# Kernel tuning notes

Hardware: AMD Instinct MI355X
Metric: run time of the kernel (lower is better)

The kernel has to match this reference:

```python
import jax, jax.numpy as jnp
import numpy as np

# Longformer/Lawformer-style encoder: sliding-window local attention (one-sided
# window W) + G global tokens (CLS), pooler, 2-class linear head, CE loss.
B, S, D, H, DH, L, W, G = 2, 4096, 768, 12, 64, 2, 128, 1
DFF, VOCAB = 3072, 50265
NEG = -3e4  # masked-score fill, safe in fp16/bf16/fp32


def layernorm(x, g, b):
    mu = x.mean(-1, keepdims=True)
    var = ((x - mu) ** 2).mean(-1, keepdims=True)
    return (x - mu) * jax.lax.rsqrt(var + 1e-5) * g + b


def setup_inputs() -> dict:
    key = jax.random.key(0)
    ks = iter(jax.random.split(key, 64))
    nrm = lambda shape: jax.random.normal(next(ks), shape, jnp.float32) * 0.02
    inp = {
        'inputx': jax.random.randint(next(ks), (B, S), 0, VOCAB),
        'mask': jnp.ones((B, S), jnp.float32),
        'labels': jax.random.randint(next(ks), (B,), 0, 2),
        'tok_emb': nrm((VOCAB, D)),
        'pos_emb': nrm((S, D)),
        'ln_emb_g': jnp.ones((D,)), 'ln_emb_b': jnp.zeros((D,)),
        'Wq': nrm((L, D, D)), 'bq': jnp.zeros((L, D)),
        'Wk': nrm((L, D, D)), 'bk': jnp.zeros((L, D)),
        'Wv': nrm((L, D, D)), 'bv': jnp.zeros((L, D)),
        'Wqg': nrm((L, D, D)), 'bqg': jnp.zeros((L, D)),
        'Wkg': nrm((L, D, D)), 'bkg': jnp.zeros((L, D)),
        'Wvg': nrm((L, D, D)), 'bvg': jnp.zeros((L, D)),
        'Wo': nrm((L, D, D)), 'bo': jnp.zeros((L, D)),
        'ln1_g': jnp.ones((L, D)), 'ln1_b': jnp.zeros((L, D)),
        'W1': nrm((L, D, DFF)), 'b1': jnp.zeros((L, DFF)),
        'W2': nrm((L, DFF, D)), 'b2': jnp.zeros((L, D)),
        'ln2_g': jnp.ones((L, D)), 'ln2_b': jnp.zeros((L, D)),
        'Wp': nrm((D, D)), 'bp': jnp.zeros((D,)),
        'Wfc': nrm((D, 2)), 'bfc': jnp.zeros((2,)),
    }
    return inp


def reference(inputx, mask, labels, tok_emb, pos_emb, ln_emb_g, ln_emb_b,
              Wq, bq, Wk, bk, Wv, bv, Wqg, bqg, Wkg, bkg, Wvg, bvg,
              Wo, bo, ln1_g, ln1_b, W1, b1, W2, b2, ln2_g, ln2_b,
              Wp, bp, Wfc, bfc):
    x = tok_emb[inputx] + pos_emb[None]          # [B,S,D]
    x = layernorm(x, ln_emb_g, ln_emb_b)
    nb = S // W
    scale = 1.0 / np.sqrt(DH)
    # static band validity mask: query i attends keys in [i-W, i+W]
    qi = jnp.arange(W)[:, None]                   # [W,1]
    ki = jnp.arange(3 * W)[None, :]               # [1,3W]
    band = (ki >= qi) & (ki <= qi + 2 * W)        # [W,3W]
    kpos = (jnp.arange(nb)[:, None, None] - 1) * W + ki[None]  # [nb,1,3W]
    band_mask = band[None] & (kpos >= G) & (kpos < S)           # [nb,W,3W]; global keys handled separately

    def heads(t):
        return t.reshape(B, S, H, DH).transpose(0, 2, 1, 3)  # [B,H,S,DH]

    for l in range(L):
        q = heads(x @ Wq[l] + bq[l]) * scale
        k = heads(x @ Wk[l] + bk[l])
        v = heads(x @ Wv[l] + bv[l])
        qg = heads(x @ Wqg[l] + bqg[l]) * scale
        kg = heads(x @ Wkg[l] + bkg[l])
        vg = heads(x @ Wvg[l] + bvg[l])
        # --- local banded attention via 3-block gather ---
        kb = k.reshape(B, H, nb, W, DH)
        vb = v.reshape(B, H, nb, W, DH)
        kp = jnp.pad(kb, ((0, 0), (0, 0), (1, 1), (0, 0), (0, 0)))
        vp = jnp.pad(vb, ((0, 0), (0, 0), (1, 1), (0, 0), (0, 0)))
        k3 = jnp.concatenate([kp[:, :, :-2], kp[:, :, 1:-1], kp[:, :, 2:]], axis=3)  # [B,H,nb,3W,DH]
        v3 = jnp.concatenate([vp[:, :, :-2], vp[:, :, 1:-1], vp[:, :, 2:]], axis=3)
        mb = mask.reshape(B, nb, W)
        mp = jnp.pad(mb, ((0, 0), (1, 1), (0, 0)))
        m3 = jnp.concatenate([mp[:, :-2], mp[:, 1:-1], mp[:, 2:]], axis=2)  # [B,nb,3W]
        sc = jnp.einsum('bhnqd,bhnkd->bhnqk', q.reshape(B, H, nb, W, DH), k3)  # [B,H,nb,W,3W]
        ok = band_mask[None, None] & (m3[:, None, :, None, :] > 0)
        sc = jnp.where(ok, sc, NEG)
        # --- every token also attends to the G global tokens (global k/v proj) ---
        scg = jnp.einsum('bhsd,bhgd->bhsg', q, kg[:, :, :G])
        scg = jnp.where(mask[:, None, None, :G] > 0, scg, NEG)
        all_sc = jnp.concatenate([scg, sc.reshape(B, H, S, 3 * W)], axis=-1)  # [B,H,S,G+3W]
        p = jax.nn.softmax(all_sc, axis=-1)
        pg = p[..., :G]
        pb = p[..., G:].reshape(B, H, nb, W, 3 * W)
        out = jnp.einsum('bhnqk,bhnkd->bhnqd', pb, v3).reshape(B, H, S, DH)
        out = out + jnp.einsum('bhsg,bhgd->bhsd', pg, vg[:, :, :G])
        # --- global tokens: full attention over all S with global projections ---
        scf = jnp.einsum('bhgd,bhsd->bhgs', qg[:, :, :G], kg)
        scf = jnp.where(mask[:, None, None, :] > 0, scf, NEG)
        outg = jnp.einsum('bhgs,bhsd->bhgd', jax.nn.softmax(scf, axis=-1), vg)
        out = out.at[:, :, :G].set(outg)
        out = out.transpose(0, 2, 1, 3).reshape(B, S, D) @ Wo[l] + bo[l]
        x = layernorm(x + out, ln1_g[l], ln1_b[l])
        h = jax.nn.gelu(x @ W1[l] + b1[l])
        x = layernorm(x + h @ W2[l] + b2[l], ln2_g[l], ln2_b[l])
    pooled = jnp.tanh(x[:, 0] @ Wp + bp)          # pooler_output
    logits = pooled @ Wfc + bfc                   # [B,2]
    logp = jax.nn.log_softmax(logits, axis=-1)
    loss = -jnp.mean(jnp.take_along_axis(logp, labels[:, None], axis=1))
    return loss
```

## Files before the change

### kernel.cpp

```cpp
#include <hip/hip_runtime.h>
#include <hip/hip_bf16.h>
#include <math.h>

#define B_    2
#define S_    4096
#define D_    768
#define H_    12
#define DH_   64
#define L_    2
#define W_    128
#define G_    1
#define DFF_  3072
#define NEG_  (-30000.0f)
#define NROWS (B_ * S_)
#define ST5   (5 * D_)
#define QOFF  0
#define KOFF  (1 * D_)
#define VOFF  (2 * D_)
#define KGOFF (3 * D_)
#define VGOFF (4 * D_)
#define QPB   64
#define CHK   32

typedef __attribute__((ext_vector_type(8))) unsigned short bfrag;
typedef __attribute__((ext_vector_type(4))) float f32x4;

__device__ __forceinline__ unsigned short f2bf(float f) {
  __hip_bfloat16 h = __float2bfloat16(f);
  return *reinterpret_cast<unsigned short*>(&h);
}

__device__ __forceinline__ void gload16(const void* g, void* l) {
  __builtin_amdgcn_global_load_lds(
      (const __attribute__((address_space(1))) unsigned int*)g,
      (__attribute__((address_space(3))) unsigned int*)l, 16, 0, 0);
}

__device__ __forceinline__ float wave_sum(float v) {
#pragma unroll
  for (int o = 32; o > 0; o >>= 1) v += __shfl_down(v, o, 64);
  return v;
}
__device__ __forceinline__ float wave_max(float v) {
#pragma unroll
  for (int o = 32; o > 0; o >>= 1) v = fmaxf(v, __shfl_down(v, o, 64));
  return v;
}
__device__ __forceinline__ float block_sum256(float v, float* sbuf) {
  v = wave_sum(v);
  int lane = threadIdx.x & 63, wid = threadIdx.x >> 6;
  if (lane == 0) sbuf[wid] = v;
  __syncthreads();
  float r = sbuf[0] + sbuf[1] + sbuf[2] + sbuf[3];
  __syncthreads();
  return r;
}

__device__ __forceinline__ float gelu_f(float x) {
  const float c = 0.7978845608028654f;
  float x3 = x * x * x;
  return 0.5f * x * (1.0f + tanhf(c * (x + 0.044715f * x3)));
}

__global__ __launch_bounds__(256) void embed_ln_kernel(
    const int* __restrict__ inputx, const float* __restrict__ tok_emb,
    const float* __restrict__ pos_emb, const float* __restrict__ g,
    const float* __restrict__ bta, float* __restrict__ X,
    unsigned short* __restrict__ Xbf) {
  __shared__ float sbuf[4];
  int row = blockIdx.x;
  int s = row & (S_ - 1);
  int tok = inputx[row];
  const float* te = tok_emb + (size_t)tok * D_;
  const float* pe = pos_emb + (size_t)s * D_;
  float vals[3];
#pragma unroll
  for (int i = 0; i < 3; i++) {
    int d = threadIdx.x + i * 256;
    vals[i] = te[d] + pe[d];
  }
  float tot = block_sum256(vals[0] + vals[1] + vals[2], sbuf);
  float mu = tot * (1.0f / D_);
  float sq = 0.f;
#pragma unroll
  for (int i = 0; i < 3; i++) { float c = vals[i] - mu; sq += c * c; }
  float var = block_sum256(sq, sbuf) * (1.0f / D_);
  float rs = rsqrtf(var + 1e-5f);
  float* xr = X + (size_t)row * D_;
  unsigned short* xb = Xbf + (size_t)row * D_;
#pragma unroll
  for (int i = 0; i < 3; i++) {
    int d = threadIdx.x + i * 256;
    float v = (vals[i] - mu) * rs * g[d] + bta[d];
    xr[d] = v;
    xb[d] = f2bf(v);
  }
}

__global__ __launch_bounds__(256) void add_ln_kernel(
    const float* __restrict__ Xin, const float* __restrict__ T,
    const float* __restrict__ g, const float* __restrict__ bta,
    float* __restrict__ Xout, unsigned short* __restrict__ Xbf) {
  __shared__ float sbuf[4];
  int row = blockIdx.x;
  const float* xr = Xin + (size_t)row * D_;
  const float* tr = T + (size_t)row * D_;
  float vals[3];
#pragma unroll
  for (int i = 0; i < 3; i++) {
    int d = threadIdx.x + i * 256;
    vals[i] = xr[d] + tr[d];
  }
  float tot = block_sum256(vals[0] + vals[1] + vals[2], sbuf);
  float mu = tot * (1.0f / D_);
  float sq = 0.f;
#pragma unroll
  for (int i = 0; i < 3; i++) { float c = vals[i] - mu; sq += c * c; }
  float var = block_sum256(sq, sbuf) * (1.0f / D_);
  float rs = rsqrtf(var + 1e-5f);
  float* xo = Xout + (size_t)row * D_;
  unsigned short* xb = Xbf + (size_t)row * D_;
#pragma unroll
  for (int i = 0; i < 3; i++) {
    int d = threadIdx.x + i * 256;
    float v = (vals[i] - mu) * rs * g[d] + bta[d];
    xo[d] = v;
    xb[d] = f2bf(v);
  }
}

__global__ __launch_bounds__(256) void wtrans_kernel(
    const float* __restrict__ W, unsigned short* __restrict__ WT, int K, int N) {
  __shared__ float tile[32][33];
  int n0 = blockIdx.x * 32, k0 = blockIdx.y * 32;
  int tx = threadIdx.x & 31, ty = threadIdx.x >> 5;
#pragma unroll
  for (int i = 0; i < 4; i++) {
    int r = ty + i * 8;
    tile[r][tx] = W[(size_t)(k0 + r) * N + n0 + tx];
  }
  __syncthreads();
#pragma unroll
  for (int i = 0; i < 4; i++) {
    int r = ty + i * 8;
    WT[(size_t)(n0 + r) * K + k0 + tx] = f2bf(tile[tx][r]);
  }
}

__global__ __launch_bounds__(256) void bias_pack_kernel(
    const float* __restrict__ bq, const float* __restrict__ bk,
    const float* __restrict__ bv, const float* __restrict__ bkg,
    const float* __restrict__ bvg, float* __restrict__ bias5) {
  int l = blockIdx.y;
  int j = blockIdx.x * 256 + threadIdx.x;
  if (j >= ST5) return;
  int which = j / D_, r = j - which * D_;
  float v;
  switch (which) {
    case 0: v = bq[l * D_ + r]; break;
    case 1: v = bk[l * D_ + r]; break;
    case 2: v = bv[l * D_ + r]; break;
    case 3: v = bkg[l * D_ + r]; break;
    default: v = bvg[l * D_ + r]; break;
  }
  bias5[(size_t)l * ST5 + j] = v;
}

__global__ __launch_bounds__(256) void gemm_bf16_kernel(
    const unsigned short* __restrict__ A, const unsigned short* __restrict__ BT,
    const float* __restrict__ bias, float* __restrict__ C,
    unsigned short* __restrict__ Cbf, int M, int N, int K, int mode) {
  __shared__ __align__(16) unsigned short As[128 * 32];
  __shared__ __align__(16) unsigned short Bs[128 * 32];
  const int m0 = blockIdx.y * 128, n0 = blockIdx.x * 128;
  const int t = threadIdx.x;
  const int w = t >> 6, l = t & 63;
  const int wm = w >> 1, wn = w & 1;
  const int lr = l & 15, lg = l >> 4;
  f32x4 acc[4][4] = {};
  for (int k0 = 0; k0 < K; k0 += 32) {
    __syncthreads();
#pragma unroll
    for (int i = 0; i < 2; i++) {
      int idx = t + i * 256;
      int row = idx >> 2, c = idx & 3;
      gload16(&A[(size_t)(m0 + row) * K + k0 + c * 8], &As[idx * 8]);
      gload16(&BT[(size_t)(n0 + row) * K + k0 + c * 8], &Bs[idx * 8]);
    }
    __syncthreads();
    bfrag af[4], bf[4];
#pragma unroll
    for (int f = 0; f < 4; f++) {
      int ra = wm * 64 + f * 16 + lr;
      af[f] = *reinterpret_cast<const bfrag*>(&As[ra * 32 + lg * 8]);
      int rb = wn * 64 + f * 16 + lr;
      bf[f] = *reinterpret_cast<const bfrag*>(&Bs[rb * 32 + lg * 8]);
    }
#pragma unroll
    for (int mi = 0; mi < 4; mi++)
#pragma unroll
      for (int ni = 0; ni < 4; ni++)
        asm volatile("v_mfma_f32_16x16x32_bf16 %0, %1, %2, %0"
                     : "+v"(acc[mi][ni])
                     : "v"(af[mi]), "v"(bf[ni]));
  }
  asm volatile("s_nop 7\n\ts_nop 7\n\ts_nop 7");
#pragma unroll
  for (int ni = 0; ni < 4; ni++) {
    int col = n0 + wn * 64 + ni * 16 + lr;
    float bv = bias[col];
#pragma unroll
    for (int mi = 0; mi < 4; mi++) {
      int rowb = m0 + wm * 64 + mi * 16 + lg * 4;
#pragma unroll
      for (int j = 0; j < 4; j++) {
        float v = acc[mi][ni][j] + bv;
        if (mode == 1) {
          Cbf[(size_t)(rowb + j) * N + col] = f2bf(gelu_f(v));
        } else {
          C[(size_t)(rowb + j) * N + col] = v;
        }
      }
    }
  }
}

__global__ __launch_bounds__(256) void skinny_kernel(
    const float* __restrict__ Xp, size_t xstride, const float* __restrict__ W,
    const float* __restrict__ bias, float* __restrict__ out, int K, int N,
    float scale, int dotanh) {
  __shared__ float red[4][64];
  int lane = threadIdx.x & 63, sl = threadIdx.x >> 6;
  int j = blockIdx.x * 64 + lane;
  int b = blockIdx.y;
  const float* x = Xp + (size_t)b * xstride;
  int kpt = K / 4;
  float s = 0.f;
  for (int k = sl * kpt; k < (sl + 1) * kpt; k++) s += x[k] * W[(size_t)k * N + j];
  red[sl][lane] = s;
  __syncthreads();
  if (sl == 0) {
    float v = (red[0][lane] + red[1][lane] + red[2][lane] + red[3][lane] +
               bias[j]) * scale;
    if (dotanh) v = tanhf(v);
    out[(size_t)b * N + j] = v;
  }
}

__global__ __launch_bounds__(256, 4) void banded_attn_kernel(
    const float* __restrict__ X5, const float* __restrict__ mask,
    unsigned short* __restrict__ Obf) {
  __shared__ __align__(16) float k_lds[CHK * 64];
  __shared__ __align__(16) float v_lds[CHK * 64];
  __shared__ float m_lds[CHK];
  int blk = blockIdx.x, h = blockIdx.y, b = blockIdx.z;
  int nb = blk >> 1, half = blk & 1;
  int t = threadIdx.x;
  int ql = t >> 2, slice = t & 3;
  int qi = half * 64 + ql;
  int s = nb * W_ + qi;
  size_t rowb = (size_t)(b * S_ + s) * ST5 + h * DH_;

  float q[16];
#pragma unroll
  for (int i = 0; i < 4; i++) {
    float4 f = *reinterpret_cast<const float4*>(
        &X5[rowb + QOFF + slice * 16 + i * 4]);
    q[i * 4 + 0] = f.x * 0.125f;
    q[i * 4 + 1] = f.y * 0.125f;
    q[i * 4 + 2] = f.z * 0.125f;
    q[i * 4 + 3] = f.w * 0.125f;
  }

  float m = -1e30f, l = 0.f;
  float acc[16];
#pragma unroll
  for (int d = 0; d < 16; d++) acc[d] = 0.f;

  if (mask[(size_t)b * S_] > 0.f) {
    size_t gb = (size_t)(b * S_) * ST5 + h * DH_ + slice * 16;
    const float* kgp = X5 + gb + KGOFF;
    const float* vgp = X5 + gb + VGOFF;
    float sc = 0.f;
#pragma unroll
    for (int d = 0; d < 16; d++) sc += q[d] * kgp[d];
    sc += __shfl_xor(sc, 1);
    sc += __shfl_xor(sc, 2);
    m = sc;
    l = 1.f;
#pragma unroll
    for (int d = 0; d < 16; d++) acc[d] = vgp[d];
  }

  int c0 = half * 2;
  for (int c = c0; c < c0 + 10; c++) {
    int kbase = (nb - 1) * W_ + c * CHK;
    __syncthreads();
#pragma unroll
    for (int i = 0; i < 2; i++) {
      int idx = t + i * 256;
      int kr = idx >> 4, c4 = idx & 15;
      int kpos = kbase + kr;
      bool inr = (kpos >= 0) && (kpos < S_);
      size_t kvb = (size_t)(b * S_ + kpos) * ST5 + h * DH_ + c4 * 4;
      float4 kf = inr ? *reinterpret_cast<const float4*>(&X5[kvb + KOFF])
                      : make_float4(0.f, 0.f, 0.f, 0.f);
      float4 vf = inr ? *reinterpret_cast<const float4*>(&X5[kvb + VOFF])
                      : make_float4(0.f, 0.f, 0.f, 0.f);
      int ba = (kr * 256 + c4 * 16) ^ ((kr & 7) << 4);
      *reinterpret_cast<float4*>(reinterpret_cast<char*>(k_lds) + ba) = kf;
      *reinterpret_cast<float4*>(reinterpret_cast<char*>(v_lds) + ba) = vf;
    }
    if (t < CHK) {
      int kpos = kbase + t;
      m_lds[t] = (kpos >= 0 && kpos < S_) ? mask[(size_t)b * S_ + kpos] : 0.f;
    }
    __syncthreads();
    for (int j = 0; j < CHK; j++) {
      int ki = c * CHK + j;
      int kpos = kbase + j;
      bool valid = (ki >= qi) && (ki <= qi + 2 * W_) && (kpos >= G_) &&
                   (kpos < S_) && (m_lds[j] > 0.f);
      if (!valid) continue;
      float sc = 0.f;
#pragma unroll
      for (int ii = 0; ii < 4; ii++) {
        int ba = (j * 256 + (slice * 4 + ii) * 16) ^ ((j & 7) << 4);
        float4 kf = *reinterpret_cast<const float4*>(
            reinterpret_cast<const char*>(k_lds) + ba);
        sc += q[ii * 4 + 0] * kf.x + q[ii * 4 + 1] * kf.y +
              q[ii * 4 + 2] * kf.z + q[ii * 4 + 3] * kf.w;
      }
      sc += __shfl_xor(sc, 1);
      sc += __shfl_xor(sc, 2);
      float p;
      if (sc > m) {
        float r = __expf(m - sc);
        l *= r;
#pragma unroll
        for (int d = 0; d < 16; d++) acc[d] *= r;
        m = sc;
        p = 1.f;
      } else {
        p = __expf(sc - m);
      }
      l += p;
#pragma unroll
      for (int ii = 0; ii < 4; ii++) {
        int ba = (j * 256 + (slice * 4 + ii) * 16) ^ ((j & 7) << 4);
        float4 vf = *reinterpret_cast<const float4*>(
            reinterpret_cast<const char*>(v_lds) + ba);
        acc[ii * 4 + 0] += p * vf.x;
        acc[ii * 4 + 1] += p * vf.y;
        acc[ii * 4 + 2] += p * vf.z;
        acc[ii * 4 + 3] += p * vf.w;
      }
    }
  }
  float inv = 1.f / l;
  size_t ob = (size_t)(b * S_ + s) * D_ + h * DH_ + slice * 16;
#pragma unroll
  for (int i = 0; i < 4; i++) {
    ushort4 o;
    o.x = f2bf(acc[i * 4 + 0] * inv);
    o.y = f2bf(acc[i * 4 + 1] * inv);
    o.z = f2bf(acc[i * 4 + 2] * inv);
    o.w = f2bf(acc[i * 4 + 3] * inv);
    *reinterpret_cast<ushort4*>(&Obf[ob + i * 4]) = o;
  }
}

__global__ __launch_bounds__(256) void global_attn_kernel(
    const float* __restrict__ QG0, const float* __restrict__ X5,
    const float* __restrict__ mask, unsigned short* __restrict__ Obf) {
  __shared__ float sc[S_];
  __shared__ float qv[64];
  __shared__ float red[4];
  __shared__ float opart[4][64];
  int h = blockIdx.x, b = blockIdx.y;
  int t = threadIdx.x;
  if (t < 64) qv[t] = QG0[b * D_ + h * DH_ + t];
  __syncthreads();
  float lmax = -1e30f;
  for (int s = t; s < S_; s += 256) {
    const float* kp = X5 + ((size_t)(b * S_ + s)) * ST5 + KGOFF + h * DH_;
    float d0 = 0.f;
#pragma unroll
    for (int d = 0; d < 64; d++) d0 += qv[d] * kp[d];
    float v = (mask[(size_t)b * S_ + s] > 0.f) ? d0 : NEG_;
    sc[s] = v;
    lmax = fmaxf(lmax, v);
  }
  lmax = wave_max(lmax);
  int lane = t & 63, wid = t >> 6;
  if (lane == 0) red[wid] = lmax;
  __syncthreads();
  float M = fmaxf(fmaxf(red[0], red[1]), fmaxf(red[2], red[3]));
  __syncthreads();
  float ls = 0.f;
  for (int s = t; s < S_; s += 256) {
    float e = expf(sc[s] - M);
    sc[s] = e;
    ls += e;
  }
  ls = wave_sum(ls);
  if (lane == 0) red[wid] = ls;
  __syncthreads();
  float L = red[0] + red[1] + red[2] + red[3];
  {
    float o = 0.f;
    int s0 = wid * (S_ / 4), s1 = s0 + (S_ / 4);
    const float* vgp = X5 + ((size_t)(b * S_)) * ST5 + VGOFF + h * DH_ + lane;
    for (int s = s0; s < s1; s++) o += sc[s] * vgp[(size_t)s * ST5];
    opart[wid][lane] = o;
  }
  __syncthreads();
  if (t < 64) {
    float o = opart[0][t] + opart[1][t] + opart[2][t] + opart[3][t];
    Obf[((size_t)(b * S_)) * D_ + h * DH_ + t] = f2bf(o / L);
  }
}

__global__ __launch_bounds__(256) void loss_kernel(
    const float* __restrict__ pooled, const float* __restrict__ Wfc,
    const float* __restrict__ bfc, const int* __restrict__ labels,
    float* __restrict__ out) {
  __shared__ float logits[4];
  int pair = threadIdx.x >> 6, lane = threadIdx.x & 63;
  int b = pair >> 1, c = pair & 1;
  float s = 0.f;
  for (int k = lane; k < D_; k += 64) s += pooled[b * D_ + k] * Wfc[k * 2 + c];
  s = wave_sum(s);
  if (lane == 0) logits[pair] = s + bfc[c];
  __syncthreads();
  if (threadIdx.x == 0) {
    float loss = 0.f;
    for (int bb = 0; bb < B_; bb++) {
      float l0 = logits[bb * 2], l1 = logits[bb * 2 + 1];
      float mm = fmaxf(l0, l1);
      float lse = mm + logf(expf(l0 - mm) + expf(l1 - mm));
      loss += -(logits[bb * 2 + labels[bb]] - lse);
    }
    out[0] = loss * (1.0f / B_);
  }
}

extern "C" void kernel_launch(void* const* d_in, const int* in_sizes, int n_in,
                              void* d_out, int out_size, void* d_ws,
                              size_t ws_size, hipStream_t stream) {
  const int* inputx = (const int*)d_in[0];
  const float* mask = (const float*)d_in[1];
  const int* labels = (const int*)d_in[2];
  const float* tok_emb = (const float*)d_in[3];
  const float* pos_emb = (const float*)d_in[4];
  const float* ln_emb_g = (const float*)d_in[5];
  const float* ln_emb_b = (const float*)d_in[6];
  const float* Wq = (const float*)d_in[7];
  const float* bq = (const float*)d_in[8];
  const float* Wk = (const float*)d_in[9];
  const float* bk = (const float*)d_in[10];
  const float* Wv = (const float*)d_in[11];
  const float* bv = (const float*)d_in[12];
  const float* Wqg = (const float*)d_in[13];
  const float* bqg = (const float*)d_in[14];
  const float* Wkg = (const float*)d_in[15];
  const float* bkg = (const float*)d_in[16];
  const float* Wvg = (const float*)d_in[17];
  const float* bvg = (const float*)d_in[18];
  const float* Wo = (const float*)d_in[19];
  const float* bo = (const float*)d_in[20];
  const float* ln1_g = (const float*)d_in[21];
  const float* ln1_b = (const float*)d_in[22];
  const float* W1 = (const float*)d_in[23];
  const float* b1 = (const float*)d_in[24];
  const float* W2 = (const float*)d_in[25];
  const float* b2 = (const float*)d_in[26];
  const float* ln2_g = (const float*)d_in[27];
  const float* ln2_b = (const float*)d_in[28];
  const float* Wp = (const float*)d_in[29];
  const float* bp = (const float*)d_in[30];
  const float* Wfc = (const float*)d_in[31];
  const float* bfc = (const float*)d_in[32];

  const size_t NB = (size_t)B_ * S_ * D_;
  const size_t NB5 = NB * 5;
  float* ws = (float*)d_ws;
  float* X = ws;
  float* QKV5 = X + NB;
  float* Tb = QKV5 + NB5;
  float* QG0 = Tb + NB;
  float* pooled = QG0 + (size_t)B_ * D_;
  float* bias5 = pooled + (size_t)B_ * D_;
  unsigned short* Xbf = (unsigned short*)(bias5 + (size_t)L_ * ST5);
  unsigned short* Obf = Xbf + NB;
  unsigned short* WTbf = Obf + NB;
  unsigned short* Hbf = (unsigned short*)QKV5;

  const size_t DD = (size_t)D_ * D_;
  const size_t DF = (size_t)D_ * DFF_;
  const size_t PLS = 6 * DD + 2 * DF;

  for (int l = 0; l < L_; l++) {
    unsigned short* wt = WTbf + l * PLS;
    wtrans_kernel<<<dim3(24, 24), 256, 0, stream>>>(Wq + l * DD, wt + 0 * DD, D_, D_);
    wtrans_kernel<<<dim3(24, 24), 256, 0, stream>>>(Wk + l * DD, wt + 1 * DD, D_, D_);
    wtrans_kernel<<<dim3(24, 24), 256, 0, stream>>>(Wv + l * DD, wt + 2 * DD, D_, D_);
    wtrans_kernel<<<dim3(24, 24), 256, 0, stream>>>(Wkg + l * DD, wt + 3 * DD, D_, D_);
    wtrans_kernel<<<dim3(24, 24), 256, 0, stream>>>(Wvg + l * DD, wt + 4 * DD, D_, D_);
    wtrans_kernel<<<dim3(24, 24), 256, 0, stream>>>(Wo + l * DD, wt + 5 * DD, D_, D_);
    wtrans_kernel<<<dim3(96, 24), 256, 0, stream>>>(W1 + l * DF, wt + 6 * DD, D_, DFF_);
    wtrans_kernel<<<dim3(24, 96), 256, 0, stream>>>(W2 + l * DF, wt + 6 * DD + DF, DFF_, D_);
  }
  bias_pack_kernel<<<dim3(15, L_), 256, 0, stream>>>(bq, bk, bv, bkg, bvg, bias5);

  embed_ln_kernel<<<NROWS, 256, 0, stream>>>(inputx, tok_emb, pos_emb, ln_emb_g,
                                             ln_emb_b, X, Xbf);

  dim3 qkv_g(ST5 / 128, NROWS / 128);
  dim3 gemm_g(D_ / 128, NROWS / 128);
  dim3 ffn1_g(DFF_ / 128, NROWS / 128);
  dim3 attn_g(S_ / QPB, H_, B_);
  dim3 gl_g(H_, B_);
  dim3 sk_g(D_ / 64, B_);

  for (int l = 0; l < L_; l++) {
    unsigned short* wt = WTbf + l * PLS;
    gemm_bf16_kernel<<<qkv_g, 256, 0, stream>>>(Xbf, wt, bias5 + (size_t)l * ST5,
                                                QKV5, nullptr, NROWS, ST5, D_, 0);
    skinny_kernel<<<sk_g, 256, 0, stream>>>(X, (size_t)S_ * D_, Wqg + l * DD,
                                            bqg + (size_t)l * D_, QG0, D_, D_,
                                            0.125f, 0);
    banded_attn_kernel<<<attn_g, 256, 0, stream>>>(QKV5, mask, Obf);
    global_attn_kernel<<<gl_g, 256, 0, stream>>>(QG0, QKV5, mask, Obf);
    gemm_bf16_kernel<<<gemm_g, 256, 0, stream>>>(Obf, wt + 5 * DD, bo + (size_t)l * D_,
                                                 Tb, nullptr, NROWS, D_, D_, 0);
    add_ln_kernel<<<NROWS, 256, 0, stream>>>(X, Tb, ln1_g + (size_t)l * D_,
                                             ln1_b + (size_t)l * D_, X, Xbf);
    gemm_bf16_kernel<<<ffn1_g, 256, 0, stream>>>(Xbf, wt + 6 * DD, b1 + (size_t)l * DFF_,
                                                 nullptr, Hbf, NROWS, DFF_, D_, 1);
    gemm_bf16_kernel<<<gemm_g, 256, 0, stream>>>(Hbf, wt + 6 * DD + DF,
                                                 b2 + (size_t)l * D_, Tb, nullptr,
                                                 NROWS, D_, DFF_, 0);
    add_ln_kernel<<<NROWS, 256, 0, stream>>>(X, Tb, ln2_g + (size_t)l * D_,
                                             ln2_b + (size_t)l * D_, X, Xbf);
  }
  skinny_kernel<<<sk_g, 256, 0, stream>>>(X, (size_t)S_ * D_, Wp, bp, pooled,
                                          D_, D_, 1.0f, 1);
  loss_kernel<<<1, 256, 0, stream>>>(pooled, Wfc, bfc, labels, (float*)d_out);
}
```

Baseline: 1.848 ms.

## Rewrite banded attention with bf16 MFMA flash-style tiles

Replaces the scalar per-key online-softmax banded attention with a kernel in which each wave computes 16 queries against 64-key chunks using v_mfma_f32_16x16x32_bf16 for both QK^T and PV. Q, K and transposed V are staged as bf16 in padded LDS, and the global token is handled as an extra chunk. Softmax statistics are updated per chunk with row-wide shuffles. This trades fp32 scalar FMAs and per-key branches for matrix-core throughput, at the cost of bf16 rounding of Q/K/V/P and some wasted work on masked band entries.

Result: faster. 1.537 ms (-16.8%).

```diff
diff --git a/kernel.cpp b/kernel.cpp
--- a/kernel.cpp
+++ b/kernel.cpp
@@ -19,10 +19,10 @@
 #define VOFF  (2 * D_)
 #define KGOFF (3 * D_)
 #define VGOFF (4 * D_)
-#define QPB   64
-#define CHK   32
+#define LDSW  68
 
 typedef __attribute__((ext_vector_type(8))) unsigned short bfrag;
+typedef __attribute__((ext_vector_type(4))) unsigned short u16x4;
 typedef __attribute__((ext_vector_type(4))) float f32x4;
 
 __device__ __forceinline__ unsigned short f2bf(float f) {
@@ -34,6 +34,14 @@
   __builtin_amdgcn_global_load_lds(
       (const __attribute__((address_space(1))) unsigned int*)g,
       (__attribute__((address_space(3))) unsigned int*)l, 16, 0, 0);
+}
+
+__device__ __forceinline__ bfrag ldsfrag(const unsigned short* base, int row,
+                                         int f, int lg) {
+  const u16x4* p =
+      reinterpret_cast<const u16x4*>(base + row * LDSW + f * 32 + lg * 8);
+  u16x4 a = p[0], c = p[1];
+  return __builtin_shufflevector(a, c, 0, 1, 2, 3, 4, 5, 6, 7);
 }
 
 __device__ __forceinline__ float wave_sum(float v) {
@@ -247,127 +255,202 @@
   }
 }
 
-__global__ __launch_bounds__(256, 4) void banded_attn_kernel(
+__global__ __launch_bounds__(256) void banded_attn_mfma_kernel(
     const float* __restrict__ X5, const float* __restrict__ mask,
     unsigned short* __restrict__ Obf) {
-  __shared__ __align__(16) float k_lds[CHK * 64];
-  __shared__ __align__(16) float v_lds[CHK * 64];
-  __shared__ float m_lds[CHK];
-  int blk = blockIdx.x, h = blockIdx.y, b = blockIdx.z;
-  int nb = blk >> 1, half = blk & 1;
-  int t = threadIdx.x;
-  int ql = t >> 2, slice = t & 3;
-  int qi = half * 64 + ql;
-  int s = nb * W_ + qi;
-  size_t rowb = (size_t)(b * S_ + s) * ST5 + h * DH_;
-
-  float q[16];
-#pragma unroll
-  for (int i = 0; i < 4; i++) {
-    float4 f = *reinterpret_cast<const float4*>(
-        &X5[rowb + QOFF + slice * 16 + i * 4]);
-    q[i * 4 + 0] = f.x * 0.125f;
-    q[i * 4 + 1] = f.y * 0.125f;
-    q[i * 4 + 2] = f.z * 0.125f;
-    q[i * 4 + 3] = f.w * 0.125f;
-  }
-
-  float m = -1e30f, l = 0.f;
-  float acc[16];
-#pragma unroll
-  for (int d = 0; d < 16; d++) acc[d] = 0.f;
-
-  if (mask[(size_t)b * S_] > 0.f) {
-    size_t gb = (size_t)(b * S_) * ST5 + h * DH_ + slice * 16;
-    const float* kgp = X5 + gb + KGOFF;
-    const float* vgp = X5 + gb + VGOFF;
-    float sc = 0.f;
-#pragma unroll
-    for (int d = 0; d < 16; d++) sc += q[d] * kgp[d];
-    sc += __shfl_xor(sc, 1);
-    sc += __shfl_xor(sc, 2);
-    m = sc;
-    l = 1.f;
-#pragma unroll
-    for (int d = 0; d < 16; d++) acc[d] = vgp[d];
-  }
-
-  int c0 = half * 2;
-  for (int c = c0; c < c0 + 10; c++) {
-    int kbase = (nb - 1) * W_ + c * CHK;
+  __shared__ __align__(16) unsigned short k_lds[64 * LDSW];
+  __shared__ __align__(16) unsigned short vt_lds[64 * LDSW];
+  __shared__ __align__(16) unsigned short q_lds[64 * LDSW];
+  __shared__ float m_lds[64];
+  const int blk = blockIdx.x, h = blockIdx.y, b = blockIdx.z;
+  const int nb = blk >> 1, half = blk & 1;
+  const int t = threadIdx.x, w = t >> 6, l = t & 63;
+  const int lr = l & 15, lg = l >> 4;
+  const int qbase = half * 64 + w * 16;
+  const float maskG = mask[(size_t)b * S_];
+
+  {
+    int qr = t >> 2, dq = (t & 3) * 16;
+    size_t src =
+        (size_t)(b * S_ + nb * W_ + half * 64 + qr) * ST5 + QOFF + h * DH_;
+#pragma unroll
+    for (int i = 0; i < 4; i++) {
+      int d0 = dq + i * 4;
+      float4 f = *reinterpret_cast<const float4*>(&X5[src + d0]);
+      u16x4 p;
+      p[0] = f2bf(f.x * 0.125f);
+      p[1] = f2bf(f.y * 0.125f);
+      p[2] = f2bf(f.z * 0.125f);
+      p[3] = f2bf(f.w * 0.125f);
+      *reinterpret_cast<u16x4*>(&q_lds[qr * LDSW + d0]) = p;
+    }
+  }
+  __syncthreads();
+  bfrag qf[2];
+#pragma unroll
+  for (int f = 0; f < 2; f++) qf[f] = ldsfrag(q_lds, w * 16 + lr, f, lg);
+
+  f32x4 o[4] = {};
+  float mrun[4], lrun[4];
+#pragma unroll
+  for (int j = 0; j < 4; j++) { mrun[j] = -3.0e38f; lrun[j] = 0.f; }
+
+  for (int cc = 0; cc < 6; cc++) {
+    const bool isg = (cc == 0);
+    const int cband = half + cc - 1;
+    const int kbase = isg ? 0 : ((nb - 1) * W_ + cband * 64);
     __syncthreads();
-#pragma unroll
-    for (int i = 0; i < 2; i++) {
-      int idx = t + i * 256;
-      int kr = idx >> 4, c4 = idx & 15;
-      int kpos = kbase + kr;
-      bool inr = (kpos >= 0) && (kpos < S_);
-      size_t kvb = (size_t)(b * S_ + kpos) * ST5 + h * DH_ + c4 * 4;
-      float4 kf = inr ? *reinterpret_cast<const float4*>(&X5[kvb + KOFF])
-                      : make_float4(0.f, 0.f, 0.f, 0.f);
-      float4 vf = inr ? *reinterpret_cast<const float4*>(&X5[kvb + VOFF])
-                      : make_float4(0.f, 0.f, 0.f, 0.f);
-      int ba = (kr * 256 + c4 * 16) ^ ((kr & 7) << 4);
-      *reinterpret_cast<float4*>(reinterpret_cast<char*>(k_lds) + ba) = kf;
-      *reinterpret_cast<float4*>(reinterpret_cast<char*>(v_lds) + ba) = vf;
-    }
-    if (t < CHK) {
-      int kpos = kbase + t;
-      m_lds[t] = (kpos >= 0 && kpos < S_) ? mask[(size_t)b * S_ + kpos] : 0.f;
+    {
+      int key = t >> 2, dq = (t & 3) * 16;
+      if (!isg) {
+        int kpos = kbase + key;
+        bool inr = (kpos >= 0) && (kpos < S_);
+        size_t kvb = (size_t)(b * S_ + kpos) * ST5 + h * DH_;
+#pragma unroll
+        for (int i = 0; i < 4; i++) {
+          int d0 = dq + i * 4;
+          float4 kf4 = inr ? *reinterpret_cast<const float4*>(&X5[kvb + KOFF + d0])
+                           : make_float4(0.f, 0.f, 0.f, 0.f);
+          float4 vf4 = inr ? *reinterpret_cast<const float4*>(&X5[kvb + VOFF + d0])
+                           : make_float4(0.f, 0.f, 0.f, 0.f);
+          u16x4 kp;
+          kp[0] = f2bf(kf4.x); kp[1] = f2bf(kf4.y);
+          kp[2] = f2bf(kf4.z); kp[3] = f2bf(kf4.w);
+          *reinterpret_cast<u16x4*>(&k_lds[key * LDSW + d0]) = kp;
+          vt_lds[(d0 + 0) * LDSW + key] = f2bf(vf4.x);
+          vt_lds[(d0 + 1) * LDSW + key] = f2bf(vf4.y);
+          vt_lds[(d0 + 2) * LDSW + key] = f2bf(vf4.z);
+          vt_lds[(d0 + 3) * LDSW + key] = f2bf(vf4.w);
+        }
+      } else {
+        size_t gb = (size_t)(b * S_) * ST5 + h * DH_;
+#pragma unroll
+        for (int i = 0; i < 4; i++) {
+          int d0 = dq + i * 4;
+          float4 kf4 = (key == 0)
+                           ? *reinterpret_cast<const float4*>(&X5[gb + KGOFF + d0])
+                           : make_float4(0.f, 0.f, 0.f, 0.f);
+          float4 vf4 = (key == 0)
+                           ? *reinterpret_cast<const float4*>(&X5[gb + VGOFF + d0])
+                           : make_float4(0.f, 0.f, 0.f, 0.f);
+          u16x4 kp;
+          kp[0] = f2bf(kf4.x); kp[1] = f2bf(kf4.y);
+          kp[2] = f2bf(kf4.z); kp[3] = f2bf(kf4.w);
+          *reinterpret_cast<u16x4*>(&k_lds[key * LDSW + d0]) = kp;
+          vt_lds[(d0 + 0) * LDSW + key] = f2bf(vf4.x);
+          vt_lds[(d0 + 1) * LDSW + key] = f2bf(vf4.y);
+          vt_lds[(d0 + 2) * LDSW + key] = f2bf(vf4.z);
+          vt_lds[(d0 + 3) * LDSW + key] = f2bf(vf4.w);
+        }
+      }
+      if (t < 64) {
+        int kpos = kbase + t;
+        m_lds[t] = (!isg && kpos >= 0 && kpos < S_)
+                       ? mask[(size_t)b * S_ + kpos] : 0.f;
+      }
     }
     __syncthreads();
-    for (int j = 0; j < CHK; j++) {
-      int ki = c * CHK + j;
-      int kpos = kbase + j;
-      bool valid = (ki >= qi) && (ki <= qi + 2 * W_) && (kpos >= G_) &&
-                   (kpos < S_) && (m_lds[j] > 0.f);
-      if (!valid) continue;
-      float sc = 0.f;
-#pragma unroll
-      for (int ii = 0; ii < 4; ii++) {
-        int ba = (j * 256 + (slice * 4 + ii) * 16) ^ ((j & 7) << 4);
-        float4 kf = *reinterpret_cast<const float4*>(
-            reinterpret_cast<const char*>(k_lds) + ba);
-        sc += q[ii * 4 + 0] * kf.x + q[ii * 4 + 1] * kf.y +
-              q[ii * 4 + 2] * kf.z + q[ii * 4 + 3] * kf.w;
-      }
-      sc += __shfl_xor(sc, 1);
-      sc += __shfl_xor(sc, 2);
-      float p;
-      if (sc > m) {
-        float r = __expf(m - sc);
-        l *= r;
-#pragma unroll
-        for (int d = 0; d < 16; d++) acc[d] *= r;
-        m = sc;
-        p = 1.f;
+    f32x4 s[4] = {};
+#pragma unroll
+    for (int f = 0; f < 2; f++)
+#pragma unroll
+      for (int nt = 0; nt < 4; nt++) {
+        bfrag kf = ldsfrag(k_lds, nt * 16 + lr, f, lg);
+        asm volatile("v_mfma_f32_16x16x32_bf16 %0, %1, %2, %0"
+                     : "+v"(s[nt]) : "v"(qf[f]), "v"(kf));
+      }
+    asm volatile("s_nop 7\n\ts_nop 7\n\ts_nop 7");
+    float mnew[4];
+#pragma unroll
+    for (int j = 0; j < 4; j++) mnew[j] = mrun[j];
+    unsigned okrow[4] = {0u, 0u, 0u, 0u};
+#pragma unroll
+    for (int nt = 0; nt < 4; nt++) {
+      int keyl = nt * 16 + lr;
+      bool okk;
+      int ki;
+      if (isg) {
+        okk = (keyl == 0) && (maskG > 0.f);
+        ki = 0;
       } else {
-        p = __expf(sc - m);
-      }
-      l += p;
-#pragma unroll
-      for (int ii = 0; ii < 4; ii++) {
-        int ba = (j * 256 + (slice * 4 + ii) * 16) ^ ((j & 7) << 4);
-        float4 vf = *reinterpret_cast<const float4*>(
-            reinterpret_cast<const char*>(v_lds) + ba);
-        acc[ii * 4 + 0] += p * vf.x;
-        acc[ii * 4 + 1] += p * vf.y;
-        acc[ii * 4 + 2] += p * vf.z;
-        acc[ii * 4 + 3] += p * vf.w;
-      }
-    }
-  }
-  float inv = 1.f / l;
-  size_t ob = (size_t)(b * S_ + s) * D_ + h * DH_ + slice * 16;
-#pragma unroll
-  for (int i = 0; i < 4; i++) {
-    ushort4 o;
-    o.x = f2bf(acc[i * 4 + 0] * inv);
-    o.y = f2bf(acc[i * 4 + 1] * inv);
-    o.z = f2bf(acc[i * 4 + 2] * inv);
-    o.w = f2bf(acc[i * 4 + 3] * inv);
-    *reinterpret_cast<ushort4*>(&Obf[ob + i * 4]) = o;
-  }
+        int kpos = kbase + keyl;
+        okk = (kpos >= G_) && (kpos < S_) && (m_lds[keyl] > 0.f);
+        ki = cband * 64 + keyl;
+      }
+#pragma unroll
+      for (int j = 0; j < 4; j++) {
+        int qi = qbase + lg * 4 + j;
+        bool ok = okk && (isg || ((ki >= qi) && (ki <= qi + 2 * W_)));
+        if (ok) {
+          mnew[j] = fmaxf(mnew[j], s[nt][j]);
+          okrow[j] |= (1u << nt);
+        }
+      }
+    }
+#pragma unroll
+    for (int j = 0; j < 4; j++) {
+      float v = mnew[j];
+      v = fmaxf(v, __shfl_xor(v, 1));
+      v = fmaxf(v, __shfl_xor(v, 2));
+      v = fmaxf(v, __shfl_xor(v, 4));
+      v = fmaxf(v, __shfl_xor(v, 8));
+      mnew[j] = v;
+    }
+    float fac[4], psum[4];
+#pragma unroll
+    for (int j = 0; j < 4; j++) {
+      fac[j] = __expf(mrun[j] - mnew[j]);
+      psum[j] = 0.f;
+    }
+#pragma unroll
+    for (int nt = 0; nt < 4; nt++)
+#pragma unroll
+      for (int j = 0; j < 4; j++) {
+        float p = ((okrow[j] >> nt) & 1u) ? __expf(s[nt][j] - mnew[j]) : 0.f;
+        s[nt][j] = p;
+        psum[j] += p;
+      }
+#pragma unroll
+    for (int j = 0; j < 4; j++) {
+      float v = psum[j];
+      v += __shfl_xor(v, 1);
+      v += __shfl_xor(v, 2);
+      v += __shfl_xor(v, 4);
+      v += __shfl_xor(v, 8);
+      lrun[j] = lrun[j] * fac[j] + v;
+      mrun[j] = mnew[j];
+    }
+#pragma unroll
+    for (int nt = 0; nt < 4; nt++)
+#pragma unroll
+      for (int j = 0; j < 4; j++) o[nt][j] *= fac[j];
+#pragma unroll
+    for (int nt = 0; nt < 4; nt++)
+#pragma unroll
+      for (int j = 0; j < 4; j++)
+        q_lds[(w * 16 + lg * 4 + j) * LDSW + nt * 16 + lr] = f2bf(s[nt][j]);
+    __syncthreads();
+    bfrag pf[2];
+#pragma unroll
+    for (int f = 0; f < 2; f++) pf[f] = ldsfrag(q_lds, w * 16 + lr, f, lg);
+#pragma unroll
+    for (int f = 0; f < 2; f++)
+#pragma unroll
+      for (int nt = 0; nt < 4; nt++) {
+        bfrag vtf = ldsfrag(vt_lds, nt * 16 + lr, f, lg);
+        asm volatile("v_mfma_f32_16x16x32_bf16 %0, %1, %2, %0"
+                     : "+v"(o[nt]) : "v"(pf[f]), "v"(vtf));
+      }
+  }
+  asm volatile("s_nop 7\n\ts_nop 7\n\ts_nop 7");
+#pragma unroll
+  for (int nt = 0; nt < 4; nt++)
+#pragma unroll
+    for (int j = 0; j < 4; j++) {
+      int srow = nb * W_ + qbase + lg * 4 + j;
+      float val = o[nt][j] / lrun[j];
+      Obf[(size_t)(b * S_ + srow) * D_ + h * DH_ + nt * 16 + lr] = f2bf(val);
+    }
 }
 
 __global__ __launch_bounds__(256) void global_attn_kernel(
@@ -519,7 +602,7 @@
   dim3 qkv_g(ST5 / 128, NROWS / 128);
   dim3 gemm_g(D_ / 128, NROWS / 128);
   dim3 ffn1_g(DFF_ / 128, NROWS / 128);
-  dim3 attn_g(S_ / QPB, H_, B_);
+  dim3 attn_g(S_ / 64, H_, B_);
   dim3 gl_g(H_, B_);
   dim3 sk_g(D_ / 64, B_);
 
@@ -530,7 +613,7 @@
     skinny_kernel<<<sk_g, 256, 0, stream>>>(X, (size_t)S_ * D_, Wqg + l * DD,
                                             bqg + (size_t)l * D_, QG0, D_, D_,
                                             0.125f, 0);
-    banded_attn_kernel<<<attn_g, 256, 0, stream>>>(QKV5, mask, Obf);
+    banded_attn_mfma_kernel<<<attn_g, 256, 0, stream>>>(QKV5, mask, Obf);
     global_attn_kernel<<<gl_g, 256, 0, stream>>>(QG0, QKV5, mask, Obf);
     gemm_bf16_kernel<<<gemm_g, 256, 0, stream>>>(Obf, wt + 5 * DD, bo + (size_t)l * D_,
                                                  Tb, nullptr, NROWS, D_, D_, 0);
```
